# Optimization experiments

Measured on AMD Instinct MI355X. Metric: run time of the kernel, lower is better.

## Reference

```python
import jax, jax.numpy as jnp
import numpy as np

N, D, C = 16384, 64, 128
MARGIN = 1.0
EPS_NORM = 1e-6   # F.normalize eps
EPS_PD = 1e-6     # F.pairwise_distance eps (added to the difference elementwise)


def setup_inputs() -> dict:
    key = jax.random.key(0)
    embeddings = jax.random.normal(key, (N, D), dtype=jnp.float32)
    labels = (jnp.arange(N) % C).astype(jnp.int32).reshape(N, 1)
    # deterministic valid positive: same label (i % C), different index
    pos_idx = ((jnp.arange(N) + C) % N).astype(jnp.int32)
    return {"embeddings": embeddings, "labels": labels, "pos_idx": pos_idx}


def reference(embeddings, labels, pos_idx):
    # L2-normalize rows (torch F.normalize: x / max(||x||, eps))
    nrm = jnp.linalg.norm(embeddings, axis=1, keepdims=True)
    e = embeddings / jnp.maximum(nrm, EPS_NORM)

    lab = labels[:, 0]
    # torch pairwise_distance computes ||x1 - x2 + eps||_2, eps added per element:
    # ||xi - xj + eps||^2 = ||xi||^2 + ||xj||^2 - 2 xi.xj + 2*eps*(sum(xi)-sum(xj)) + D*eps^2
    sq = jnp.sum(e * e, axis=1)          # [N]
    s = jnp.sum(e, axis=1)               # [N]
    gram = e @ e.T                        # [N, N]
    d2 = (sq[:, None] + sq[None, :] - 2.0 * gram
          + 2.0 * EPS_PD * (s[:, None] - s[None, :]) + D * EPS_PD * EPS_PD)
    d2 = jnp.maximum(d2, 0.0)
    dist = jnp.sqrt(jnp.maximum(d2, 1e-12))  # guard sqrt grad at 0

    # one positive per anchor: squared distance
    pos_loss = jnp.sum(d2[jnp.arange(N), pos_idx])

    # all negatives per anchor: hinge^2 on (margin - dist)
    neg_mask = lab[:, None] != lab[None, :]
    hinge = jnp.maximum(MARGIN - dist, 0.0)
    neg_loss = jnp.sum(jnp.where(neg_mask, hinge * hinge, 0.0))

    n_comparisons = N + jnp.sum(neg_mask)
    return (pos_loss + neg_loss) / n_comparisons.astype(jnp.float32)
```

## Files before the change

kernel.cpp:

```cpp
#include <hip/hip_runtime.h>
#include <hip/hip_bf16.h>

#define NN 16384
#define DD 64
#define TT 128
#define NTRI ((TT*(TT+1))/2)
#define NBLK 1024
#define NPOSB (NN/4)
#define SCREEN_T 0.49f

constexpr float F_EPS_PD   = 1e-6f;
constexpr float F_EPS_NORM = 1e-6f;

using bf16x8 = __attribute__((ext_vector_type(8))) short;
using f32x4  = __attribute__((ext_vector_type(4))) float;
typedef __attribute__((address_space(1))) const unsigned int gu32_t;
typedef __attribute__((address_space(3))) unsigned int       lu32_t;

__device__ __forceinline__ float wave_sum_f(float v) {
    #pragma unroll
    for (int o = 32; o >= 1; o >>= 1) v += __shfl_xor(v, o);
    return v;
}

__device__ __forceinline__ int tri_off(int t) { return t * TT - (t * (t - 1)) / 2; }

__global__ __launch_bounds__(256) void norm_kernel(
    const float* __restrict__ emb, const int* __restrict__ pidx,
    float* __restrict__ u, float* __restrict__ vc,
    __hip_bfloat16* __restrict__ ebf, float* __restrict__ posP) {
    int w    = threadIdx.x >> 6;
    int row  = blockIdx.x * 4 + w;
    int lane = threadIdx.x & 63;
    int j    = pidx[row];
    float x  = emb[(size_t)row * DD + lane];
    float xj = emb[(size_t)j   * DD + lane];

    float n2  = wave_sum_f(x * x);
    float sx  = wave_sum_f(x);
    float n2j = wave_sum_f(xj * xj);
    float sxj = wave_sum_f(xj);
    float dot = wave_sum_f(x * xj);

    float m  = fmaxf(sqrtf(n2),  F_EPS_NORM);
    float mj = fmaxf(sqrtf(n2j), F_EPS_NORM);
    ebf[(size_t)row * DD + lane] = __float2bfloat16(x / m);

    __shared__ float spos[4];
    if (lane == 0) {
        float sq  = n2 / (m * m);
        float sqj = n2j / (mj * mj);
        float s   = sx / m;
        float sj  = sxj / mj;
        float g   = dot / (m * mj);
        u[row]  = sq + 2.0f * F_EPS_PD * s;
        vc[row] = sq - 2.0f * F_EPS_PD * s + (float)DD * F_EPS_PD * F_EPS_PD;
        float d2p = sq + sqj - 2.0f * g + 2.0f * F_EPS_PD * (s - sj)
                  + (float)DD * F_EPS_PD * F_EPS_PD;
        spos[w] = fmaxf(d2p, 0.0f);
    }
    __syncthreads();
    if (threadIdx.x == 0)
        posP[blockIdx.x] = spos[0] + spos[1] + spos[2] + spos[3];
}

__global__ __launch_bounds__(256, 4) void pair_kernel(
    const short* __restrict__ ebf, const float* __restrict__ u,
    const float* __restrict__ vc, const int* __restrict__ lab,
    float* __restrict__ negP) {
    __shared__ short lbs[2][8192];
    int tid  = threadIdx.x;
    int w    = tid >> 6;
    int lane = tid & 63;
    int lrow = lane & 15, lkh = lane >> 4;

    int ks = (int)(((long long)blockIdx.x * NTRI) / NBLK);
    int ke = (int)(((long long)(blockIdx.x + 1) * NTRI) / NBLK);

    int ti = (int)(128.5f - sqrtf(128.5f * 128.5f - 2.0f * (float)ks));
    ti = ti < 0 ? 0 : (ti > TT - 1 ? TT - 1 : ti);
    while (tri_off(ti) > ks) --ti;
    while (ti < TT - 1 && tri_off(ti + 1) <= ks) ++ti;
    int tj = ti + (ks - tri_off(ti));

    int srr  = (w & 1) * 64 + lane;
    int wsel = w >> 1;

    bf16x8 a00, a01, a10, a11;
    float hacc = 0.0f;
    int cur = 0;

    {
        const short* bt = ebf + (size_t)tj * (128 * DD);
        #pragma unroll
        for (int q = 0; q < 4; ++q) {
            int chunk = 2 * q + wsel;
            __builtin_amdgcn_global_load_lds(
                (gu32_t*)(const void*)(bt + (size_t)srr * DD + chunk * 8),
                (lu32_t*)(void*)&lbs[0][q * 2048 + w * 512], 16, 0, 0);
        }
        const short* ab = ebf + (size_t)(ti * 128 + w * 32 + lrow) * DD + lkh * 8;
        a00 = *(const bf16x8*)(ab);
        a01 = *(const bf16x8*)(ab + 32);
        a10 = *(const bf16x8*)(ab + 16 * DD);
        a11 = *(const bf16x8*)(ab + 16 * DD + 32);
    }
    __syncthreads();

    for (int k = ks; k < ke; ++k) {
        int nti = ti, ntj = tj + 1;
        bool more = (k + 1 < ke);
        if (more) {
            if (ntj == TT) { nti = ti + 1; ntj = nti; }
            const short* bt = ebf + (size_t)ntj * (128 * DD);
            #pragma unroll
            for (int q = 0; q < 4; ++q) {
                int chunk = 2 * q + wsel;
                __builtin_amdgcn_global_load_lds(
                    (gu32_t*)(const void*)(bt + (size_t)srr * DD + chunk * 8),
                    (lu32_t*)(void*)&lbs[cur ^ 1][q * 2048 + w * 512], 16, 0, 0);
            }
        }

        int bi = ti * 128 + w * 32;
        int bj = tj * 128;
        const short* lb = lbs[cur];
        float hp = 0.0f;
        #pragma unroll
        for (int t = 0; t < 8; ++t) {
            bf16x8 b0 = *(const bf16x8*)&lb[lkh * 1024 + (t * 16 + lrow) * 8];
            bf16x8 b1 = *(const bf16x8*)&lb[(lkh + 4) * 1024 + (t * 16 + lrow) * 8];
            f32x4 c0 = {0.f, 0.f, 0.f, 0.f};
            c0 = __builtin_amdgcn_mfma_f32_16x16x32_bf16(a00, b0, c0, 0, 0, 0);
            c0 = __builtin_amdgcn_mfma_f32_16x16x32_bf16(a01, b1, c0, 0, 0, 0);
            f32x4 c1 = {0.f, 0.f, 0.f, 0.f};
            c1 = __builtin_amdgcn_mfma_f32_16x16x32_bf16(a10, b0, c1, 0, 0, 0);
            c1 = __builtin_amdgcn_mfma_f32_16x16x32_bf16(a11, b1, c1, 0, 0, 0);

            float m0 = fmaxf(fmaxf(c0[0], c0[1]), fmaxf(c0[2], c0[3]));
            float m1 = fmaxf(fmaxf(c1[0], c1[1]), fmaxf(c1[2], c1[3]));
            if (__any(fmaxf(m0, m1) > SCREEN_T)) {
                int j = bj + t * 16 + lrow;
                float vj = vc[j]; int lj = lab[j];
                #pragma unroll
                for (int r = 0; r < 4; ++r) {
                    int i0 = bi + lkh * 4 + r;
                    float d2a = fmaf(-2.0f, c0[r], u[i0] + vj);
                    float d2b = fmaf(-2.0f, c1[r], u[i0 + 16] + vj);
                    float da = sqrtf(fmaxf(d2a, 1e-12f));
                    float db = sqrtf(fmaxf(d2b, 1e-12f));
                    float ha = fmaxf(1.0f - da, 0.0f);
                    float hb = fmaxf(1.0f - db, 0.0f);
                    if (lab[i0]      != lj) hp = fmaf(ha, ha, hp);
                    if (lab[i0 + 16] != lj) hp = fmaf(hb, hb, hp);
                }
            }
        }
        hacc += (ti == tj) ? hp : hp + hp;

        __syncthreads();
        cur ^= 1;
        if (more && nti != ti) {
            const short* ab = ebf + (size_t)(nti * 128 + w * 32 + lrow) * DD + lkh * 8;
            a00 = *(const bf16x8*)(ab);
            a01 = *(const bf16x8*)(ab + 32);
            a10 = *(const bf16x8*)(ab + 16 * DD);
            a11 = *(const bf16x8*)(ab + 16 * DD + 32);
        }
        ti = nti; tj = ntj;
    }

    hacc = wave_sum_f(hacc);
    float* sred = (float*)lbs;
    if (lane == 0) sred[w] = hacc;
    __syncthreads();
    if (tid == 0)
        negP[blockIdx.x] = sred[0] + sred[1] + sred[2] + sred[3];
}

__global__ __launch_bounds__(256) void reduce_kernel(
    const float* __restrict__ posP, const float* __restrict__ negP,
    const int* __restrict__ lab, float* __restrict__ out) {
    __shared__ unsigned int hist[1024];
    int t = threadIdx.x;
    for (int i = t; i < 1024; i += 256) hist[i] = 0u;
    __syncthreads();
    for (int i = t; i < NN; i += 256) {
        int l = lab[i];
        l = l < 0 ? 0 : (l > 1023 ? 1023 : l);
        atomicAdd(&hist[l], 1u);
    }
    __syncthreads();

    float ps = 0.f, ns = 0.f;
    unsigned int sqc = 0u;
    for (int i = t; i < NPOSB; i += 256) ps += posP[i];
    for (int i = t; i < NBLK; i += 256) ns += negP[i];
    for (int i = t; i < 1024; i += 256) { unsigned int h = hist[i]; sqc += h * h; }

    ps = wave_sum_f(ps);
    ns = wave_sum_f(ns);
    #pragma unroll
    for (int o = 32; o >= 1; o >>= 1) sqc += __shfl_xor(sqc, o);

    __shared__ float sp[4], sn[4];
    __shared__ unsigned int sc[4];
    int w = t >> 6, lane = t & 63;
    if (lane == 0) { sp[w] = ps; sn[w] = ns; sc[w] = sqc; }
    __syncthreads();
    if (t == 0) {
        float pos = sp[0] + sp[1] + sp[2] + sp[3];
        float neg = sn[0] + sn[1] + sn[2] + sn[3];
        unsigned long long s2 = (unsigned long long)sc[0] + sc[1] + sc[2] + sc[3];
        unsigned long long nneg = (unsigned long long)NN * NN - s2;
        float ncomp = (float)((unsigned long long)NN + nneg);
        out[0] = (pos + neg) / ncomp;
    }
}

extern "C" void kernel_launch(void* const* d_in, const int* in_sizes, int n_in,
                              void* d_out, int out_size, void* d_ws, size_t ws_size,
                              hipStream_t stream) {
    const float* emb = (const float*)d_in[0];
    const int* lab   = (const int*)d_in[1];
    const int* pidx  = (const int*)d_in[2];
    float* out = (float*)d_out;
    char* ws = (char*)d_ws;
    float*          u    = (float*)(ws);
    float*          vc   = (float*)(ws + 65536);
    __hip_bfloat16* ebf  = (__hip_bfloat16*)(ws + 131072);
    float*          posP = (float*)(ws + 2228224);
    float*          negP = (float*)(ws + 2244608);

    norm_kernel<<<NPOSB, 256, 0, stream>>>(emb, pidx, u, vc, ebf, posP);
    pair_kernel<<<NBLK, 256, 0, stream>>>((const short*)ebf, u, vc, lab, negP);
    reduce_kernel<<<1, 256, 0, stream>>>(posP, negP, lab, out);
}
```

Before: 57.43 us.

## Use 256-row anchor bands per block to raise B-tile reuse

```diff
diff --git a/kernel.cpp b/kernel.cpp
--- a/kernel.cpp
+++ b/kernel.cpp
@@ -4,7 +4,8 @@
 #define NN 16384
 #define DD 64
 #define TT 128
-#define NTRI ((TT*(TT+1))/2)
+#define NB 64
+#define NUNITS 4160
 #define NBLK 1024
 #define NPOSB (NN/4)
 #define SCREEN_T 0.49f
@@ -23,7 +24,7 @@
     return v;
 }
 
-__device__ __forceinline__ int tri_off(int t) { return t * TT - (t * (t - 1)) / 2; }
+__device__ __forceinline__ int band_off(int I) { return I * (129 - I); }
 
 __global__ __launch_bounds__(256) void norm_kernel(
     const float* __restrict__ emb, const int* __restrict__ pidx,
@@ -74,19 +75,20 @@
     int lane = tid & 63;
     int lrow = lane & 15, lkh = lane >> 4;
 
-    int ks = (int)(((long long)blockIdx.x * NTRI) / NBLK);
-    int ke = (int)(((long long)(blockIdx.x + 1) * NTRI) / NBLK);
-
-    int ti = (int)(128.5f - sqrtf(128.5f * 128.5f - 2.0f * (float)ks));
-    ti = ti < 0 ? 0 : (ti > TT - 1 ? TT - 1 : ti);
-    while (tri_off(ti) > ks) --ti;
-    while (ti < TT - 1 && tri_off(ti + 1) <= ks) ++ti;
-    int tj = ti + (ks - tri_off(ti));
+    int ks = (int)(((long long)blockIdx.x * NUNITS) / NBLK);
+    int ke = (int)(((long long)(blockIdx.x + 1) * NUNITS) / NBLK);
+
+    int I = (int)((129.0f - sqrtf(16641.0f - 4.0f * (float)ks)) * 0.5f);
+    I = I < 0 ? 0 : (I > NB - 1 ? NB - 1 : I);
+    while (band_off(I) > ks) --I;
+    while (I < NB - 1 && band_off(I + 1) <= ks) ++I;
+    int tj = 2 * I + (ks - band_off(I));
 
     int srr  = (w & 1) * 64 + lane;
     int wsel = w >> 1;
 
-    bf16x8 a00, a01, a10, a11;
+    bf16x8 a[4][2];
+    int rowbase = I * 256 + w * 64;
     float hacc = 0.0f;
     int cur = 0;
 
@@ -99,19 +101,20 @@
                 (gu32_t*)(const void*)(bt + (size_t)srr * DD + chunk * 8),
                 (lu32_t*)(void*)&lbs[0][q * 2048 + w * 512], 16, 0, 0);
         }
-        const short* ab = ebf + (size_t)(ti * 128 + w * 32 + lrow) * DD + lkh * 8;
-        a00 = *(const bf16x8*)(ab);
-        a01 = *(const bf16x8*)(ab + 32);
-        a10 = *(const bf16x8*)(ab + 16 * DD);
-        a11 = *(const bf16x8*)(ab + 16 * DD + 32);
+        #pragma unroll
+        for (int s = 0; s < 4; ++s) {
+            const short* ab = ebf + (size_t)(rowbase + 16 * s + lrow) * DD + lkh * 8;
+            a[s][0] = *(const bf16x8*)(ab);
+            a[s][1] = *(const bf16x8*)(ab + 32);
+        }
     }
     __syncthreads();
 
     for (int k = ks; k < ke; ++k) {
-        int nti = ti, ntj = tj + 1;
+        int nI = I, ntj = tj + 1;
         bool more = (k + 1 < ke);
         if (more) {
-            if (ntj == TT) { nti = ti + 1; ntj = nti; }
+            if (ntj == TT) { nI = I + 1; ntj = 2 * nI; }
             const short* bt = ebf + (size_t)ntj * (128 * DD);
             #pragma unroll
             for (int q = 0; q < 4; ++q) {
@@ -122,52 +125,59 @@
             }
         }
 
-        int bi = ti * 128 + w * 32;
-        int bj = tj * 128;
-        const short* lb = lbs[cur];
-        float hp = 0.0f;
-        #pragma unroll
-        for (int t = 0; t < 8; ++t) {
-            bf16x8 b0 = *(const bf16x8*)&lb[lkh * 1024 + (t * 16 + lrow) * 8];
-            bf16x8 b1 = *(const bf16x8*)&lb[(lkh + 4) * 1024 + (t * 16 + lrow) * 8];
-            f32x4 c0 = {0.f, 0.f, 0.f, 0.f};
-            c0 = __builtin_amdgcn_mfma_f32_16x16x32_bf16(a00, b0, c0, 0, 0, 0);
-            c0 = __builtin_amdgcn_mfma_f32_16x16x32_bf16(a01, b1, c0, 0, 0, 0);
-            f32x4 c1 = {0.f, 0.f, 0.f, 0.f};
-            c1 = __builtin_amdgcn_mfma_f32_16x16x32_bf16(a10, b0, c1, 0, 0, 0);
-            c1 = __builtin_amdgcn_mfma_f32_16x16x32_bf16(a11, b1, c1, 0, 0, 0);
-
-            float m0 = fmaxf(fmaxf(c0[0], c0[1]), fmaxf(c0[2], c0[3]));
-            float m1 = fmaxf(fmaxf(c1[0], c1[1]), fmaxf(c1[2], c1[3]));
-            if (__any(fmaxf(m0, m1) > SCREEN_T)) {
-                int j = bj + t * 16 + lrow;
-                float vj = vc[j]; int lj = lab[j];
+        int rt = 2 * I + (w >> 1);
+        float wgt = (tj == rt) ? 1.0f : ((tj > rt) ? 2.0f : 0.0f);
+        if (wgt != 0.0f) {
+            int bj = tj * 128;
+            const short* lb = lbs[cur];
+            float hp = 0.0f;
+            #pragma unroll
+            for (int t = 0; t < 8; ++t) {
+                bf16x8 b0 = *(const bf16x8*)&lb[lkh * 1024 + (t * 16 + lrow) * 8];
+                bf16x8 b1 = *(const bf16x8*)&lb[(lkh + 4) * 1024 + (t * 16 + lrow) * 8];
+                f32x4 c[4];
                 #pragma unroll
-                for (int r = 0; r < 4; ++r) {
-                    int i0 = bi + lkh * 4 + r;
-                    float d2a = fmaf(-2.0f, c0[r], u[i0] + vj);
-                    float d2b = fmaf(-2.0f, c1[r], u[i0 + 16] + vj);
-                    float da = sqrtf(fmaxf(d2a, 1e-12f));
-                    float db = sqrtf(fmaxf(d2b, 1e-12f));
-                    float ha = fmaxf(1.0f - da, 0.0f);
-                    float hb = fmaxf(1.0f - db, 0.0f);
-                    if (lab[i0]      != lj) hp = fmaf(ha, ha, hp);
-                    if (lab[i0 + 16] != lj) hp = fmaf(hb, hb, hp);
+                for (int s = 0; s < 4; ++s) {
+                    f32x4 z = {0.f, 0.f, 0.f, 0.f};
+                    z = __builtin_amdgcn_mfma_f32_16x16x32_bf16(a[s][0], b0, z, 0, 0, 0);
+                    z = __builtin_amdgcn_mfma_f32_16x16x32_bf16(a[s][1], b1, z, 0, 0, 0);
+                    c[s] = z;
+                }
+                float mx = fmaxf(fmaxf(c[0][0], c[0][1]), fmaxf(c[0][2], c[0][3]));
+                mx = fmaxf(mx, fmaxf(fmaxf(c[1][0], c[1][1]), fmaxf(c[1][2], c[1][3])));
+                mx = fmaxf(mx, fmaxf(fmaxf(c[2][0], c[2][1]), fmaxf(c[2][2], c[2][3])));
+                mx = fmaxf(mx, fmaxf(fmaxf(c[3][0], c[3][1]), fmaxf(c[3][2], c[3][3])));
+                if (__any(mx > SCREEN_T)) {
+                    int j = bj + t * 16 + lrow;
+                    float vj = vc[j]; int lj = lab[j];
+                    #pragma unroll
+                    for (int s = 0; s < 4; ++s) {
+                        #pragma unroll
+                        for (int r = 0; r < 4; ++r) {
+                            int i0 = rowbase + 16 * s + lkh * 4 + r;
+                            float d2 = fmaf(-2.0f, c[s][r], u[i0] + vj);
+                            float d  = sqrtf(fmaxf(d2, 1e-12f));
+                            float h  = fmaxf(1.0f - d, 0.0f);
+                            if (lab[i0] != lj) hp = fmaf(h, h, hp);
+                        }
+                    }
                 }
             }
-        }
-        hacc += (ti == tj) ? hp : hp + hp;
+            hacc = fmaf(wgt, hp, hacc);
+        }
 
         __syncthreads();
         cur ^= 1;
-        if (more && nti != ti) {
-            const short* ab = ebf + (size_t)(nti * 128 + w * 32 + lrow) * DD + lkh * 8;
-            a00 = *(const bf16x8*)(ab);
-            a01 = *(const bf16x8*)(ab + 32);
-            a10 = *(const bf16x8*)(ab + 16 * DD);
-            a11 = *(const bf16x8*)(ab + 16 * DD + 32);
-        }
-        ti = nti; tj = ntj;
+        if (more && nI != I) {
+            rowbase = nI * 256 + w * 64;
+            #pragma unroll
+            for (int s = 0; s < 4; ++s) {
+                const short* ab = ebf + (size_t)(rowbase + 16 * s + lrow) * DD + lkh * 8;
+                a[s][0] = *(const bf16x8*)(ab);
+                a[s][1] = *(const bf16x8*)(ab + 32);
+            }
+        }
+        I = nI; tj = ntj;
     }
 
     hacc = wave_sum_f(hacc);
@@ -185,16 +195,23 @@
     int t = threadIdx.x;
     for (int i = t; i < 1024; i += 256) hist[i] = 0u;
     __syncthreads();
-    for (int i = t; i < NN; i += 256) {
-        int l = lab[i];
-        l = l < 0 ? 0 : (l > 1023 ? 1023 : l);
-        atomicAdd(&hist[l], 1u);
+    const int4* lab4 = (const int4*)lab;
+    for (int i = t; i < NN / 4; i += 256) {
+        int4 v = lab4[i];
+        atomicAdd(&hist[v.x & 1023], 1u);
+        atomicAdd(&hist[v.y & 1023], 1u);
+        atomicAdd(&hist[v.z & 1023], 1u);
+        atomicAdd(&hist[v.w & 1023], 1u);
     }
     __syncthreads();
 
     float ps = 0.f, ns = 0.f;
     unsigned int sqc = 0u;
-    for (int i = t; i < NPOSB; i += 256) ps += posP[i];
+    const float4* posP4 = (const float4*)posP;
+    for (int i = t; i < NPOSB / 4; i += 256) {
+        float4 v = posP4[i];
+        ps += (v.x + v.y) + (v.z + v.w);
+    }
     for (int i = t; i < NBLK; i += 256) ns += negP[i];
     for (int i = t; i < 1024; i += 256) { unsigned int h = hist[i]; sqc += h * h; }
 
```

Result: slower. 61.62 us (+7.3%).
